# Optimization experiments

Measured on AMD Instinct MI355X. Metric: run time of the kernel, lower is better.

The kernel has to match this reference:

```python
import jax, jax.numpy as jnp
import numpy as np

N = 5000
NFEAT = 512
NHID = 64
NHEADS = 8
NCLASS = 40
ALPHA = 0.2  # leaky relu slope
NEG_INF = -9e15


def setup_inputs() -> dict:
    key = jax.random.key(0)
    ks = jax.random.split(key, 12)
    x = jax.random.normal(ks[0], (N, NFEAT), dtype=jnp.float32)
    # binary adjacency, ~32 avg degree, with self loops
    adj = (jax.random.uniform(ks[1], (N, N)) < (32.0 / N)).astype(jnp.float32)
    adj = jnp.maximum(adj, jnp.eye(N, dtype=jnp.float32))
    s = 1.0 / np.sqrt(NFEAT)
    W_h = jax.random.uniform(ks[2], (NHEADS, NFEAT, NHID), minval=-s, maxval=s, dtype=jnp.float32)
    a_h = jax.random.uniform(ks[3], (NHEADS, 2 * NHID), minval=-s, maxval=s, dtype=jnp.float32)
    s2 = 1.0 / np.sqrt(NHID * NHEADS)
    W_o = jax.random.uniform(ks[4], (NHID * NHEADS, NHID), minval=-s2, maxval=s2, dtype=jnp.float32)
    a_o = jax.random.uniform(ks[5], (2 * NHID,), minval=-s2, maxval=s2, dtype=jnp.float32)
    s3 = 1.0 / np.sqrt(NHID)
    fc1_w = jax.random.uniform(ks[6], (NHID, 200), minval=-s3, maxval=s3, dtype=jnp.float32)
    fc1_b = jax.random.uniform(ks[7], (200,), minval=-s3, maxval=s3, dtype=jnp.float32)
    s4 = 1.0 / np.sqrt(200)
    fc2_w = jax.random.uniform(ks[8], (200, NCLASS), minval=-s4, maxval=s4, dtype=jnp.float32)
    fc2_b = jax.random.uniform(ks[9], (NCLASS,), minval=-s4, maxval=s4, dtype=jnp.float32)
    return {"x": x, "adj": adj, "W_h": W_h, "a_h": a_h, "W_o": W_o, "a_o": a_o,
            "fc1_w": fc1_w, "fc1_b": fc1_b, "fc2_w": fc2_w, "fc2_b": fc2_b}


def _masked_attention(e, adj):
    # e: [..., N, N]; mask where adj == 0, then row softmax
    e = jnp.where(adj > 0, e, NEG_INF)
    return jax.nn.softmax(e, axis=-1)


def reference(x, adj, W_h, a_h, W_o, a_o, fc1_w, fc1_b, fc2_w, fc2_b):
    # ---- multi-head GAT layer (concat=True), eval mode (dropout off) ----
    Wh = jnp.einsum('nf,hfo->hno', x, W_h)                 # [H, N, nhid]
    f1 = jnp.einsum('hno,ho->hn', Wh, a_h[:, :NHID])       # [H, N]
    f2 = jnp.einsum('hno,ho->hn', Wh, a_h[:, NHID:])       # [H, N]
    e = jax.nn.leaky_relu(f1[:, :, None] + f2[:, None, :], ALPHA)  # [H, N, N]
    att = _masked_attention(e, adj[None, :, :])
    h = jnp.einsum('hnm,hmo->hno', att, Wh)                # [H, N, nhid]
    h1 = jax.nn.elu(h).transpose(1, 0, 2).reshape(N, NHEADS * NHID)  # concat heads

    # ---- output GAT layer (concat=False) ----
    Wh2 = h1 @ W_o                                         # [N, nhid]
    g1 = Wh2 @ a_o[:NHID]                                  # [N]
    g2 = Wh2 @ a_o[NHID:]                                  # [N]
    e2 = jax.nn.leaky_relu(g1[:, None] + g2[None, :], ALPHA)
    att2 = _masked_attention(e2, adj)
    h2 = att2 @ Wh2                                        # [N, nhid]

    # ---- MLP head ----
    h3 = jax.nn.elu(h2 @ fc1_w + fc1_b)
    return h3 @ fc2_w + fc2_b                              # [N, nclass]
```

## Files before the change

### kernel.cpp

```cpp
#include <hip/hip_runtime.h>

typedef unsigned short u16;
typedef unsigned int u32;
typedef __bf16 bf16_t;
typedef __bf16 bf16x8 __attribute__((ext_vector_type(8)));
typedef float f32x4 __attribute__((ext_vector_type(4)));

#define NN 5000
#define NF 512
#define NH 64
#define HEADS 8
#define NCLS 40
#define CAP 128
#define LRELU 0.2f

__device__ __forceinline__ bool adj_is_bf16(const void* adj) {
    return ((*(const u32*)adj) & 0xFFFFu) != 0u;
}
__device__ __forceinline__ u16 rne_bf16(float f) {
    u32 u = __float_as_uint(f);
    u += 0x7FFFu + ((u >> 16) & 1u);
    return (u16)(u >> 16);
}
__device__ __forceinline__ float up_bf16(u16 h) {
    return __uint_as_float((u32)h << 16);
}

#define CVT_AB_BLKS 344
__global__ __launch_bounds__(256) void prep(const void* __restrict__ x, const void* __restrict__ W_h,
                                            const void* __restrict__ adj,
                                            const void* a_h, const void* W_o, const void* a_o,
                                            const void* f1w, const void* f1b,
                                            const void* f2w, const void* f2b,
                                            u16* __restrict__ xc, u16* __restrict__ whc,
                                            float* a_hc, float* W_oc, float* a_oc,
                                            float* f1wc, float* f1bc, float* f2wc, float* f2bc,
                                            int* __restrict__ nbr, int* __restrict__ deg) {
    const bool isb = adj_is_bf16(adj);
    const int b = blockIdx.x;
    if (b < NN) {
        __shared__ int cnt;
        if (threadIdx.x == 0) cnt = 0;
        __syncthreads();
        int* nrow = nbr + (size_t)b * CAP;
        if (isb) {
            const uint4* row4 = (const uint4*)((const u16*)adj + (size_t)b * NN);
            for (int c = threadIdx.x; c < NN / 8; c += 256) {
                uint4 v = row4[c];
                u32 w[4] = {v.x, v.y, v.z, v.w};
                int base = c * 8;
                #pragma unroll
                for (int q = 0; q < 4; ++q) {
                    if (w[q] & 0xFFFFu) { int p = atomicAdd(&cnt, 1); if (p < CAP) nrow[p] = base + 2 * q; }
                    if (w[q] >> 16)     { int p = atomicAdd(&cnt, 1); if (p < CAP) nrow[p] = base + 2 * q + 1; }
                }
            }
        } else {
            const uint4* row4 = (const uint4*)((const float*)adj + (size_t)b * NN);
            for (int c = threadIdx.x; c < NN / 4; c += 256) {
                uint4 v = row4[c];
                u32 w[4] = {v.x, v.y, v.z, v.w};
                int base = c * 4;
                #pragma unroll
                for (int q = 0; q < 4; ++q)
                    if (w[q]) { int p = atomicAdd(&cnt, 1); if (p < CAP) nrow[p] = base + q; }
            }
        }
        __syncthreads();
        if (threadIdx.x == 0) deg[b] = cnt < CAP ? cnt : CAP;
    } else if (b < NN + CVT_AB_BLKS) {
        const int total = NN * NF + HEADS * NF * NH;
        for (int i = (b - NN) * 256 + threadIdx.x; i < total; i += CVT_AB_BLKS * 256) {
            const void* src; u16* dst; int off;
            if (i < NN * NF) { src = x; dst = xc; off = i; }
            else             { src = W_h; dst = whc; off = i - NN * NF; }
            dst[off] = isb ? ((const u16*)src)[off] : rne_bf16(((const float*)src)[off]);
        }
    } else {
        const int s0 = HEADS * 2 * NH, s1 = HEADS * NH * NH, s2 = 2 * NH,
                  s3 = NH * 200, s4 = 200, s5 = 200 * NCLS, s6 = NCLS;
        const int total = s0 + s1 + s2 + s3 + s4 + s5 + s6;
        for (int i = (b - NN - CVT_AB_BLKS) * 256 + threadIdx.x; i < total; i += 8 * 256) {
            const void* src; float* dst; int off = i;
            if (off < s0) { src = a_h; dst = a_hc; }
            else if ((off -= s0) < s1) { src = W_o;  dst = W_oc; }
            else if ((off -= s1) < s2) { src = a_o;  dst = a_oc; }
            else if ((off -= s2) < s3) { src = f1w;  dst = f1wc; }
            else if ((off -= s3) < s4) { src = f1b;  dst = f1bc; }
            else if ((off -= s4) < s5) { src = f2w;  dst = f2wc; }
            else { off -= s5;           src = f2b;  dst = f2bc; }
            dst[off] = isb ? up_bf16(((const u16*)src)[off]) : ((const float*)src)[off];
        }
    }
}

__global__ __launch_bounds__(256) void gemm1_f(const bf16_t* __restrict__ x,
                                               const bf16_t* __restrict__ W_h,
                                               const float* __restrict__ a_h,
                                               float* __restrict__ Wh,
                                               float* __restrict__ f1,
                                               float* __restrict__ f2) {
    const int lane = threadIdx.x & 63;
    const int wid  = threadIdx.x >> 6;
    const int rg = blockIdx.x;
    const int h  = blockIdx.y;
    const int quad = lane >> 4;
    const int lr   = lane & 15;
    const int kq   = quad * 8;
    const int nCol = wid * 16 + lr;
    const bf16_t* Bh = W_h + (size_t)h * NF * NH;
    __shared__ float f1s[4][64], f2s[4][64];

    bf16x8 bfrag[16];
    #pragma unroll
    for (int s = 0; s < 16; ++s) {
        bf16x8 bb;
        #pragma unroll
        for (int j = 0; j < 8; ++j) bb[j] = Bh[(s * 32 + kq + j) * NH + nCol];
        bfrag[s] = bb;
    }
    const float a1c = a_h[h * 128 + nCol];
    const float a2c = a_h[h * 128 + NH + nCol];

    for (int t = 0; t < 4; ++t) {
        const int rb = rg * 64 + t * 16;
        int row  = rb + lr;
        int rowc = row < NN ? row : NN - 1;
        const bf16_t* xp = x + (size_t)rowc * NF + kq;
        f32x4 acc = {0.f, 0.f, 0.f, 0.f};
        #pragma unroll
        for (int s = 0; s < 16; ++s) {
            bf16x8 a = *(const bf16x8*)(xp + s * 32);
            acc = __builtin_amdgcn_mfma_f32_16x16x32_bf16(a, bfrag[s], acc, 0, 0, 0);
        }
        #pragma unroll
        for (int r = 0; r < 4; ++r) {
            int gr = rb + quad * 4 + r;
            if (gr < NN) Wh[((size_t)(h * NN + gr)) * NH + nCol] = acc[r];
            float p1 = acc[r] * a1c, p2 = acc[r] * a2c;
            #pragma unroll
            for (int o = 8; o; o >>= 1) { p1 += __shfl_xor(p1, o); p2 += __shfl_xor(p2, o); }
            if (lr == 0) { f1s[wid][t * 16 + quad * 4 + r] = p1; f2s[wid][t * 16 + quad * 4 + r] = p2; }
        }
    }
    __syncthreads();
    if (wid == 0) {
        int gr = rg * 64 + lane;
        if (gr < NN) {
            f1[h * NN + gr] = f1s[0][lane] + f1s[1][lane] + f1s[2][lane] + f1s[3][lane];
            f2[h * NN + gr] = f2s[0][lane] + f2s[1][lane] + f2s[2][lane] + f2s[3][lane];
        }
    }
}

__global__ __launch_bounds__(256) void agg1(const float* __restrict__ Wh,
                                            const float* __restrict__ f1,
                                            const float* __restrict__ f2,
                                            const int* __restrict__ nbr,
                                            const int* __restrict__ deg,
                                            float* __restrict__ h1) {
    const int lane = threadIdx.x & 63;
    const int wid  = threadIdx.x >> 6;
    const int gw = blockIdx.x * 4 + wid;
    const int h = gw / NN;
    const int n = gw - h * NN;
    __shared__ float s_alpha[4][CAP];
    __shared__ int   s_nbr[4][CAP];
    const int d = deg[n];
    const int* nb = nbr + (size_t)n * CAP;
    const float f1n = f1[gw];
    const float* f2h = f2 + (size_t)h * NN;

    float mx = -INFINITY;
    for (int j = lane; j < d; j += 64) {
        int m = nb[j];
        s_nbr[wid][j] = m;
        float e = f1n + f2h[m];
        e = e > 0.f ? e : LRELU * e;
        s_alpha[wid][j] = e;
        mx = fmaxf(mx, e);
    }
    #pragma unroll
    for (int o = 32; o; o >>= 1) mx = fmaxf(mx, __shfl_xor(mx, o));
    float sm = 0.f;
    for (int j = lane; j < d; j += 64) {
        float p = expf(s_alpha[wid][j] - mx);
        s_alpha[wid][j] = p;
        sm += p;
    }
    #pragma unroll
    for (int o = 32; o; o >>= 1) sm += __shfl_xor(sm, o);

    float acc0 = 0.f, acc1 = 0.f;
    const float* WhL = Wh + (size_t)h * NN * NH + lane;
    int j = 0;
    for (; j + 2 <= d; j += 2) {
        acc0 += s_alpha[wid][j]     * WhL[(size_t)s_nbr[wid][j]     * NH];
        acc1 += s_alpha[wid][j + 1] * WhL[(size_t)s_nbr[wid][j + 1] * NH];
    }
    if (j < d) acc0 += s_alpha[wid][j] * WhL[(size_t)s_nbr[wid][j] * NH];
    float hv = (acc0 + acc1) / sm;
    hv = hv > 0.f ? hv : expf(hv) - 1.f;
    h1[(size_t)n * (HEADS * NH) + h * NH + lane] = hv;
}

__global__ __launch_bounds__(256) void gemm2_4(const float* __restrict__ h1,
                                               const float* __restrict__ W_o,
                                               const float* __restrict__ a_o,
                                               float* __restrict__ Wh2,
                                               float* __restrict__ g1,
                                               float* __restrict__ g2) {
    const int t = threadIdx.x;
    const int n0 = blockIdx.x * 4;
    __shared__ float sh[4 * 512];
    __shared__ float ps[4][4][64];
    const float4* src = (const float4*)(h1 + (size_t)n0 * 512);
    ((float4*)sh)[t]       = src[t];
    ((float4*)sh)[t + 256] = src[t + 256];
    __syncthreads();
    const int o = t & 63, part = t >> 6;
    float a0 = 0.f, a1 = 0.f, a2 = 0.f, a3 = 0.f;
    const float* wo = W_o + part * 128 * 64 + o;
    const float* s0 = sh + part * 128;
    #pragma unroll 4
    for (int f = 0; f < 128; ++f) {
        float w = wo[f * 64];
        a0 += s0[f] * w; a1 += s0[512 + f] * w; a2 += s0[1024 + f] * w; a3 += s0[1536 + f] * w;
    }
    ps[part][0][o] = a0; ps[part][1][o] = a1; ps[part][2][o] = a2; ps[part][3][o] = a3;
    __syncthreads();
    const int nd = t >> 6;
    float w2 = ps[0][nd][o] + ps[1][nd][o] + ps[2][nd][o] + ps[3][nd][o];
    Wh2[(size_t)(n0 + nd) * 64 + o] = w2;
    float p1 = w2 * a_o[o], p2 = w2 * a_o[64 + o];
    #pragma unroll
    for (int s = 32; s; s >>= 1) { p1 += __shfl_xor(p1, s); p2 += __shfl_xor(p2, s); }
    if (o == 0) { g1[n0 + nd] = p1; g2[n0 + nd] = p2; }
}

__global__ __launch_bounds__(256) void agg2_mlp(const float* __restrict__ Wh2,
                                                const float* __restrict__ g1,
                                                const float* __restrict__ g2,
                                                const int* __restrict__ nbr,
                                                const int* __restrict__ deg,
                                                const float* __restrict__ fc1_w,
                                                const float* __restrict__ fc1_b,
                                                const float* __restrict__ fc2_w,
                                                const float* __restrict__ fc2_b,
                                                float* __restrict__ out) {
    const int lane = threadIdx.x & 63;
    const int wid  = threadIdx.x >> 6;
    const int t = threadIdx.x;
    const int n0 = blockIdx.x * 4;
    const int n = n0 + wid;
    __shared__ float s_alpha[4][CAP];
    __shared__ int   s_nbr[4][CAP];
    __shared__ float s_h2[4][NH];
    __shared__ float s_h3[4][200];
    __shared__ float ps2[2][4][NCLS];
    const int d = deg[n];
    const int* nb = nbr + (size_t)n * CAP;
    const float gn = g1[n];

    float mx = -INFINITY;
    for (int j = lane; j < d; j += 64) {
        int m = nb[j];
        s_nbr[wid][j] = m;
        float e = gn + g2[m];
        e = e > 0.f ? e : LRELU * e;
        s_alpha[wid][j] = e;
        mx = fmaxf(mx, e);
    }
    #pragma unroll
    for (int o = 32; o; o >>= 1) mx = fmaxf(mx, __shfl_xor(mx, o));
    float sm = 0.f;
    for (int j = lane; j < d; j += 64) {
        float p = expf(s_alpha[wid][j] - mx);
        s_alpha[wid][j] = p;
        sm += p;
    }
    #pragma unroll
    for (int o = 32; o; o >>= 1) sm += __shfl_xor(sm, o);

    float acc0 = 0.f, acc1 = 0.f;
    int j = 0;
    for (; j + 2 <= d; j += 2) {
        acc0 += s_alpha[wid][j]     * Wh2[(size_t)s_nbr[wid][j]     * NH + lane];
        acc1 += s_alpha[wid][j + 1] * Wh2[(size_t)s_nbr[wid][j + 1] * NH + lane];
    }
    if (j < d) acc0 += s_alpha[wid][j] * Wh2[(size_t)s_nbr[wid][j] * NH + lane];
    s_h2[wid][lane] = (acc0 + acc1) / sm;
    __syncthreads();

    if (t < 200) {
        float b0 = 0.f, b1 = 0.f, b2 = 0.f, b3 = 0.f;
        #pragma unroll 4
        for (int f = 0; f < NH; ++f) {
            float w = fc1_w[f * 200 + t];
            b0 += s_h2[0][f] * w; b1 += s_h2[1][f] * w; b2 += s_h2[2][f] * w; b3 += s_h2[3][f] * w;
        }
        float bb = fc1_b[t];
        b0 += bb; b1 += bb; b2 += bb; b3 += bb;
        s_h3[0][t] = b0 > 0.f ? b0 : expf(b0) - 1.f;
        s_h3[1][t] = b1 > 0.f ? b1 : expf(b1) - 1.f;
        s_h3[2][t] = b2 > 0.f ? b2 : expf(b2) - 1.f;
        s_h3[3][t] = b3 > 0.f ? b3 : expf(b3) - 1.f;
    }
    __syncthreads();

    if (t < 80) {
        const int o = t % 40, fh = t / 40;
        float c0 = 0.f, c1 = 0.f, c2 = 0.f, c3 = 0.f;
        #pragma unroll 4
        for (int f = fh * 100; f < fh * 100 + 100; ++f) {
            float w = fc2_w[f * NCLS + o];
            c0 += s_h3[0][f] * w; c1 += s_h3[1][f] * w; c2 += s_h3[2][f] * w; c3 += s_h3[3][f] * w;
        }
        ps2[fh][0][o] = c0; ps2[fh][1][o] = c1; ps2[fh][2][o] = c2; ps2[fh][3][o] = c3;
    }
    __syncthreads();
    if (t < 160) {
        const int nd = t / 40, o = t % 40;
        out[(size_t)(n0 + nd) * NCLS + o] = ps2[0][nd][o] + ps2[1][nd][o] + fc2_b[o];
    }
}

extern "C" void kernel_launch(void* const* d_in, const int* in_sizes, int n_in,
                              void* d_out, int out_size, void* d_ws, size_t ws_size,
                              hipStream_t stream) {
    const void* x     = d_in[0];
    const void* adj   = d_in[1];
    const void* W_h   = d_in[2];
    const void* a_h   = d_in[3];
    const void* W_o   = d_in[4];
    const void* a_o   = d_in[5];
    const void* fc1_w = d_in[6];
    const void* fc1_b = d_in[7];
    const void* fc2_w = d_in[8];
    const void* fc2_b = d_in[9];
    float* out = (float*)d_out;

    char* ws = (char*)d_ws;
    int*   nbr   = (int*)(ws + 0);
    int*   deg   = (int*)(ws + 2560000);
    float* Wh    = (float*)(ws + 2580000);
    float* f1    = (float*)(ws + 12820000);
    float* f2    = (float*)(ws + 12980000);
    float* h1    = (float*)(ws + 13140000);
    float* Wh2   = (float*)(ws + 23380000);
    float* g1    = (float*)(ws + 24660000);
    float* g2    = (float*)(ws + 24680000);
    u16*   xc    = (u16*)(ws + 24700000);
    u16*   whc   = (u16*)(ws + 29820000);
    float* a_hc  = (float*)(ws + 30344288);
    float* W_oc  = (float*)(ws + 30348384);
    float* a_oc  = (float*)(ws + 30479456);
    float* f1wc  = (float*)(ws + 30479968);
    float* f1bc  = (float*)(ws + 30531168);
    float* f2wc  = (float*)(ws + 30531968);
    float* f2bc  = (float*)(ws + 30563968);

    prep<<<NN + CVT_AB_BLKS + 8, 256, 0, stream>>>(x, W_h, adj, a_h, W_o, a_o,
                                                   fc1_w, fc1_b, fc2_w, fc2_b,
                                                   xc, whc, a_hc, W_oc, a_oc,
                                                   f1wc, f1bc, f2wc, f2bc, nbr, deg);
    gemm1_f<<<dim3(79, HEADS), 256, 0, stream>>>((const bf16_t*)xc, (const bf16_t*)whc,
                                                 a_hc, Wh, f1, f2);
    agg1<<<HEADS * NN / 4, 256, 0, stream>>>(Wh, f1, f2, nbr, deg, h1);
    gemm2_4<<<NN / 4, 256, 0, stream>>>(h1, W_oc, a_oc, Wh2, g1, g2);
    agg2_mlp<<<NN / 4, 256, 0, stream>>>(Wh2, g1, g2, nbr, deg,
                                         f1wc, f1bc, f2wc, f2bc, out);
}
```

Baseline: 281.9 us.

## Fuse input conversion, GEMM1 and CSR build into one kernel

```diff
diff --git a/kernel.cpp b/kernel.cpp
--- a/kernel.cpp
+++ b/kernel.cpp
@@ -14,141 +14,173 @@
 #define CAP 128
 #define LRELU 0.2f
 
+#define GEMM1B (79 * HEADS)
+#define CSR_END (GEMM1B + NN)
+#define FUSED0_GRID (CSR_END + 8)
+
 __device__ __forceinline__ bool adj_is_bf16(const void* adj) {
     return ((*(const u32*)adj) & 0xFFFFu) != 0u;
 }
-__device__ __forceinline__ u16 rne_bf16(float f) {
-    u32 u = __float_as_uint(f);
-    u += 0x7FFFu + ((u >> 16) & 1u);
-    return (u16)(u >> 16);
-}
 __device__ __forceinline__ float up_bf16(u16 h) {
     return __uint_as_float((u32)h << 16);
 }
 
-#define CVT_AB_BLKS 344
-__global__ __launch_bounds__(256) void prep(const void* __restrict__ x, const void* __restrict__ W_h,
-                                            const void* __restrict__ adj,
-                                            const void* a_h, const void* W_o, const void* a_o,
-                                            const void* f1w, const void* f1b,
-                                            const void* f2w, const void* f2b,
-                                            u16* __restrict__ xc, u16* __restrict__ whc,
-                                            float* a_hc, float* W_oc, float* a_oc,
-                                            float* f1wc, float* f1bc, float* f2wc, float* f2bc,
-                                            int* __restrict__ nbr, int* __restrict__ deg) {
+__global__ __launch_bounds__(256) void fused0(const void* __restrict__ x,
+                                              const void* __restrict__ W_h,
+                                              const void* __restrict__ adj,
+                                              const void* __restrict__ a_h,
+                                              const void* W_o, const void* a_o,
+                                              const void* f1w, const void* f1b,
+                                              const void* f2w, const void* f2b,
+                                              float* __restrict__ Wh,
+                                              float* __restrict__ f1,
+                                              float* __restrict__ f2,
+                                              int* __restrict__ nbr, int* __restrict__ deg,
+                                              float* W_oc, float* a_oc,
+                                              float* f1wc, float* f1bc, float* f2wc, float* f2bc) {
     const bool isb = adj_is_bf16(adj);
     const int b = blockIdx.x;
-    if (b < NN) {
-        __shared__ int cnt;
+    __shared__ float f1s[4][64], f2s[4][64];
+    __shared__ int cnt;
+
+    if (b < GEMM1B) {
+        const int lane = threadIdx.x & 63;
+        const int wid  = threadIdx.x >> 6;
+        const int h  = b / 79;
+        const int rg = b - h * 79;
+        const int quad = lane >> 4;
+        const int lr   = lane & 15;
+        const int kq   = quad * 8;
+        const int nCol = wid * 16 + lr;
+
+        bf16x8 bfrag[16];
+        if (isb) {
+            const bf16_t* Bh = (const bf16_t*)W_h + (size_t)h * NF * NH;
+            #pragma unroll
+            for (int s = 0; s < 16; ++s) {
+                bf16x8 bb;
+                #pragma unroll
+                for (int j = 0; j < 8; ++j) bb[j] = Bh[(s * 32 + kq + j) * NH + nCol];
+                bfrag[s] = bb;
+            }
+        } else {
+            const float* Bh = (const float*)W_h + (size_t)h * NF * NH;
+            #pragma unroll
+            for (int s = 0; s < 16; ++s) {
+                bf16x8 bb;
+                #pragma unroll
+                for (int j = 0; j < 8; ++j) bb[j] = (bf16_t)Bh[(s * 32 + kq + j) * NH + nCol];
+                bfrag[s] = bb;
+            }
+        }
+        const float a1c = isb ? up_bf16(((const u16*)a_h)[h * 128 + nCol])
+                              : ((const float*)a_h)[h * 128 + nCol];
+        const float a2c = isb ? up_bf16(((const u16*)a_h)[h * 128 + NH + nCol])
+                              : ((const float*)a_h)[h * 128 + NH + nCol];
+
+        for (int t = 0; t < 4; ++t) {
+            const int rb = rg * 64 + t * 16;
+            int row  = rb + lr;
+            int rowc = row < NN ? row : NN - 1;
+            f32x4 acc = {0.f, 0.f, 0.f, 0.f};
+            if (isb) {
+                const bf16_t* xp = (const bf16_t*)x + (size_t)rowc * NF + kq;
+                #pragma unroll
+                for (int s = 0; s < 16; ++s) {
+                    bf16x8 a = *(const bf16x8*)(xp + s * 32);
+                    acc = __builtin_amdgcn_mfma_f32_16x16x32_bf16(a, bfrag[s], acc, 0, 0, 0);
+                }
+            } else {
+                const float* xp = (const float*)x + (size_t)rowc * NF + kq;
+                #pragma unroll
+                for (int s = 0; s < 16; ++s) {
+                    float4 lo = *(const float4*)(xp + s * 32);
+                    float4 hi = *(const float4*)(xp + s * 32 + 4);
+                    bf16x8 a;
+                    a[0] = (bf16_t)lo.x; a[1] = (bf16_t)lo.y; a[2] = (bf16_t)lo.z; a[3] = (bf16_t)lo.w;
+                    a[4] = (bf16_t)hi.x; a[5] = (bf16_t)hi.y; a[6] = (bf16_t)hi.z; a[7] = (bf16_t)hi.w;
+                    acc = __builtin_amdgcn_mfma_f32_16x16x32_bf16(a, bfrag[s], acc, 0, 0, 0);
+                }
+            }
+            #pragma unroll
+            for (int r = 0; r < 4; ++r) {
+                int gr = rb + quad * 4 + r;
+                if (gr < NN) Wh[((size_t)(h * NN + gr)) * NH + nCol] = acc[r];
+                float p1 = acc[r] * a1c, p2 = acc[r] * a2c;
+                #pragma unroll
+                for (int o = 8; o; o >>= 1) { p1 += __shfl_xor(p1, o); p2 += __shfl_xor(p2, o); }
+                if (lr == 0) { f1s[wid][t * 16 + quad * 4 + r] = p1; f2s[wid][t * 16 + quad * 4 + r] = p2; }
+            }
+        }
+        __syncthreads();
+        if (wid == 0) {
+            int gr = rg * 64 + lane;
+            if (gr < NN) {
+                f1[h * NN + gr] = f1s[0][lane] + f1s[1][lane] + f1s[2][lane] + f1s[3][lane];
+                f2[h * NN + gr] = f2s[0][lane] + f2s[1][lane] + f2s[2][lane] + f2s[3][lane];
+            }
+        }
+    } else if (b < CSR_END) {
+        const int n = b - GEMM1B;
         if (threadIdx.x == 0) cnt = 0;
         __syncthreads();
-        int* nrow = nbr + (size_t)b * CAP;
+        int* nrow = nbr + (size_t)n * CAP;
         if (isb) {
-            const uint4* row4 = (const uint4*)((const u16*)adj + (size_t)b * NN);
-            for (int c = threadIdx.x; c < NN / 8; c += 256) {
-                uint4 v = row4[c];
-                u32 w[4] = {v.x, v.y, v.z, v.w};
-                int base = c * 8;
-                #pragma unroll
-                for (int q = 0; q < 4; ++q) {
-                    if (w[q] & 0xFFFFu) { int p = atomicAdd(&cnt, 1); if (p < CAP) nrow[p] = base + 2 * q; }
-                    if (w[q] >> 16)     { int p = atomicAdd(&cnt, 1); if (p < CAP) nrow[p] = base + 2 * q + 1; }
+            const uint4* row4 = (const uint4*)((const u16*)adj + (size_t)n * NN);
+            uint4 v[3];
+            #pragma unroll
+            for (int k = 0; k < 3; ++k) {
+                int c = threadIdx.x + k * 256;
+                if (c < 625) v[k] = row4[c];
+            }
+            #pragma unroll
+            for (int k = 0; k < 3; ++k) {
+                int c = threadIdx.x + k * 256;
+                if (c < 625) {
+                    u32 w[4] = {v[k].x, v[k].y, v[k].z, v[k].w};
+                    int base = c * 8;
+                    #pragma unroll
+                    for (int q = 0; q < 4; ++q) {
+                        if (w[q] & 0xFFFFu) { int p = atomicAdd(&cnt, 1); if (p < CAP) nrow[p] = base + 2 * q; }
+                        if (w[q] >> 16)     { int p = atomicAdd(&cnt, 1); if (p < CAP) nrow[p] = base + 2 * q + 1; }
+                    }
                 }
             }
         } else {
-            const uint4* row4 = (const uint4*)((const float*)adj + (size_t)b * NN);
-            for (int c = threadIdx.x; c < NN / 4; c += 256) {
-                uint4 v = row4[c];
-                u32 w[4] = {v.x, v.y, v.z, v.w};
-                int base = c * 4;
-                #pragma unroll
-                for (int q = 0; q < 4; ++q)
-                    if (w[q]) { int p = atomicAdd(&cnt, 1); if (p < CAP) nrow[p] = base + q; }
+            const uint4* row4 = (const uint4*)((const float*)adj + (size_t)n * NN);
+            uint4 v[5];
+            #pragma unroll
+            for (int k = 0; k < 5; ++k) {
+                int c = threadIdx.x + k * 256;
+                if (c < 1250) v[k] = row4[c];
+            }
+            #pragma unroll
+            for (int k = 0; k < 5; ++k) {
+                int c = threadIdx.x + k * 256;
+                if (c < 1250) {
+                    u32 w[4] = {v[k].x, v[k].y, v[k].z, v[k].w};
+                    int base = c * 4;
+                    #pragma unroll
+                    for (int q = 0; q < 4; ++q)
+                        if (w[q]) { int p = atomicAdd(&cnt, 1); if (p < CAP) nrow[p] = base + q; }
+                }
             }
         }
         __syncthreads();
-        if (threadIdx.x == 0) deg[b] = cnt < CAP ? cnt : CAP;
-    } else if (b < NN + CVT_AB_BLKS) {
-        const int total = NN * NF + HEADS * NF * NH;
-        for (int i = (b - NN) * 256 + threadIdx.x; i < total; i += CVT_AB_BLKS * 256) {
-            const void* src; u16* dst; int off;
-            if (i < NN * NF) { src = x; dst = xc; off = i; }
-            else             { src = W_h; dst = whc; off = i - NN * NF; }
-            dst[off] = isb ? ((const u16*)src)[off] : rne_bf16(((const float*)src)[off]);
-        }
+        if (threadIdx.x == 0) deg[n] = cnt < CAP ? cnt : CAP;
     } else {
-        const int s0 = HEADS * 2 * NH, s1 = HEADS * NH * NH, s2 = 2 * NH,
-                  s3 = NH * 200, s4 = 200, s5 = 200 * NCLS, s6 = NCLS;
-        const int total = s0 + s1 + s2 + s3 + s4 + s5 + s6;
-        for (int i = (b - NN - CVT_AB_BLKS) * 256 + threadIdx.x; i < total; i += 8 * 256) {
+        const int s1 = HEADS * NH * NH, s2 = 2 * NH, s3 = NH * 200, s4 = 200,
+                  s5 = 200 * NCLS, s6 = NCLS;
+        const int total = s1 + s2 + s3 + s4 + s5 + s6;
+        for (int i = (b - CSR_END) * 256 + threadIdx.x; i < total; i += 8 * 256) {
             const void* src; float* dst; int off = i;
-            if (off < s0) { src = a_h; dst = a_hc; }
-            else if ((off -= s0) < s1) { src = W_o;  dst = W_oc; }
+            if (off < s1) { src = W_o; dst = W_oc; }
             else if ((off -= s1) < s2) { src = a_o;  dst = a_oc; }
             else if ((off -= s2) < s3) { src = f1w;  dst = f1wc; }
             else if ((off -= s3) < s4) { src = f1b;  dst = f1bc; }
             else if ((off -= s4) < s5) { src = f2w;  dst = f2wc; }
             else { off -= s5;           src = f2b;  dst = f2bc; }
             dst[off] = isb ? up_bf16(((const u16*)src)[off]) : ((const float*)src)[off];
-        }
-    }
-}
-
-__global__ __launch_bounds__(256) void gemm1_f(const bf16_t* __restrict__ x,
-                                               const bf16_t* __restrict__ W_h,
-                                               const float* __restrict__ a_h,
-                                               float* __restrict__ Wh,
-                                               float* __restrict__ f1,
-                                               float* __restrict__ f2) {
-    const int lane = threadIdx.x & 63;
-    const int wid  = threadIdx.x >> 6;
-    const int rg = blockIdx.x;
-    const int h  = blockIdx.y;
-    const int quad = lane >> 4;
-    const int lr   = lane & 15;
-    const int kq   = quad * 8;
-    const int nCol = wid * 16 + lr;
-    const bf16_t* Bh = W_h + (size_t)h * NF * NH;
-    __shared__ float f1s[4][64], f2s[4][64];
-
-    bf16x8 bfrag[16];
-    #pragma unroll
-    for (int s = 0; s < 16; ++s) {
-        bf16x8 bb;
-        #pragma unroll
-        for (int j = 0; j < 8; ++j) bb[j] = Bh[(s * 32 + kq + j) * NH + nCol];
-        bfrag[s] = bb;
-    }
-    const float a1c = a_h[h * 128 + nCol];
-    const float a2c = a_h[h * 128 + NH + nCol];
-
-    for (int t = 0; t < 4; ++t) {
-        const int rb = rg * 64 + t * 16;
-        int row  = rb + lr;
-        int rowc = row < NN ? row : NN - 1;
-        const bf16_t* xp = x + (size_t)rowc * NF + kq;
-        f32x4 acc = {0.f, 0.f, 0.f, 0.f};
-        #pragma unroll
-        for (int s = 0; s < 16; ++s) {
-            bf16x8 a = *(const bf16x8*)(xp + s * 32);
-            acc = __builtin_amdgcn_mfma_f32_16x16x32_bf16(a, bfrag[s], acc, 0, 0, 0);
-        }
-        #pragma unroll
-        for (int r = 0; r < 4; ++r) {
-            int gr = rb + quad * 4 + r;
-            if (gr < NN) Wh[((size_t)(h * NN + gr)) * NH + nCol] = acc[r];
-            float p1 = acc[r] * a1c, p2 = acc[r] * a2c;
-            #pragma unroll
-            for (int o = 8; o; o >>= 1) { p1 += __shfl_xor(p1, o); p2 += __shfl_xor(p2, o); }
-            if (lr == 0) { f1s[wid][t * 16 + quad * 4 + r] = p1; f2s[wid][t * 16 + quad * 4 + r] = p2; }
-        }
-    }
-    __syncthreads();
-    if (wid == 0) {
-        int gr = rg * 64 + lane;
-        if (gr < NN) {
-            f1[h * NN + gr] = f1s[0][lane] + f1s[1][lane] + f1s[2][lane] + f1s[3][lane];
-            f2[h * NN + gr] = f2s[0][lane] + f2s[1][lane] + f2s[2][lane] + f2s[3][lane];
         }
     }
 }
@@ -350,22 +382,17 @@
     float* Wh2   = (float*)(ws + 23380000);
     float* g1    = (float*)(ws + 24660000);
     float* g2    = (float*)(ws + 24680000);
-    u16*   xc    = (u16*)(ws + 24700000);
-    u16*   whc   = (u16*)(ws + 29820000);
-    float* a_hc  = (float*)(ws + 30344288);
-    float* W_oc  = (float*)(ws + 30348384);
-    float* a_oc  = (float*)(ws + 30479456);
-    float* f1wc  = (float*)(ws + 30479968);
-    float* f1bc  = (float*)(ws + 30531168);
-    float* f2wc  = (float*)(ws + 30531968);
-    float* f2bc  = (float*)(ws + 30563968);
-
-    prep<<<NN + CVT_AB_BLKS + 8, 256, 0, stream>>>(x, W_h, adj, a_h, W_o, a_o,
-                                                   fc1_w, fc1_b, fc2_w, fc2_b,
-                                                   xc, whc, a_hc, W_oc, a_oc,
-                                                   f1wc, f1bc, f2wc, f2bc, nbr, deg);
-    gemm1_f<<<dim3(79, HEADS), 256, 0, stream>>>((const bf16_t*)xc, (const bf16_t*)whc,
-                                                 a_hc, Wh, f1, f2);
+    float* W_oc  = (float*)(ws + 24700000);
+    float* a_oc  = (float*)(ws + 24831072);
+    float* f1wc  = (float*)(ws + 24831584);
+    float* f1bc  = (float*)(ws + 24882784);
+    float* f2wc  = (float*)(ws + 24883584);
+    float* f2bc  = (float*)(ws + 24915584);
+
+    fused0<<<FUSED0_GRID, 256, 0, stream>>>(x, W_h, adj, a_h, W_o, a_o,
+                                            fc1_w, fc1_b, fc2_w, fc2_b,
+                                            Wh, f1, f2, nbr, deg,
+                                            W_oc, a_oc, f1wc, f1bc, f2wc, f2bc);
     agg1<<<HEADS * NN / 4, 256, 0, stream>>>(Wh, f1, f2, nbr, deg, h1);
     gemm2_4<<<NN / 4, 256, 0, stream>>>(h1, W_oc, a_oc, Wh2, g1, g2);
     agg2_mlp<<<NN / 4, 256, 0, stream>>>(Wh2, g1, g2, nbr, deg,
```

Measured after the change: 283.9 us. Within noise of the previous version (+0.7%).

## Scan adjacency rows per wavefront with ballot compaction and unroll gathers

Applied to the files above, without the earlier changes.

```diff
diff --git a/kernel.cpp b/kernel.cpp
--- a/kernel.cpp
+++ b/kernel.cpp
@@ -2,6 +2,7 @@
 
 typedef unsigned short u16;
 typedef unsigned int u32;
+typedef unsigned long long u64;
 typedef __bf16 bf16_t;
 typedef __bf16 bf16x8 __attribute__((ext_vector_type(8)));
 typedef float f32x4 __attribute__((ext_vector_type(4)));
@@ -14,6 +15,10 @@
 #define CAP 128
 #define LRELU 0.2f
 
+#define SCAN_BLKS 1250
+#define CVT_AB_BLKS 344
+#define PREP2_GRID (SCAN_BLKS + CVT_AB_BLKS + 8)
+
 __device__ __forceinline__ bool adj_is_bf16(const void* adj) {
     return ((*(const u32*)adj) & 0xFFFFu) != 0u;
 }
@@ -26,51 +31,88 @@
     return __uint_as_float((u32)h << 16);
 }
 
-#define CVT_AB_BLKS 344
-__global__ __launch_bounds__(256) void prep(const void* __restrict__ x, const void* __restrict__ W_h,
-                                            const void* __restrict__ adj,
-                                            const void* a_h, const void* W_o, const void* a_o,
-                                            const void* f1w, const void* f1b,
-                                            const void* f2w, const void* f2b,
-                                            u16* __restrict__ xc, u16* __restrict__ whc,
-                                            float* a_hc, float* W_oc, float* a_oc,
-                                            float* f1wc, float* f1bc, float* f2wc, float* f2bc,
-                                            int* __restrict__ nbr, int* __restrict__ deg) {
+__global__ __launch_bounds__(256) void prep2(const void* __restrict__ adj,
+                                             const void* __restrict__ x, const void* __restrict__ W_h,
+                                             const void* a_h, const void* W_o, const void* a_o,
+                                             const void* f1w, const void* f1b,
+                                             const void* f2w, const void* f2b,
+                                             int* __restrict__ nbr, int* __restrict__ deg,
+                                             u16* __restrict__ xc, u16* __restrict__ whc,
+                                             float* a_hc, float* W_oc, float* a_oc,
+                                             float* f1wc, float* f1bc, float* f2wc, float* f2bc) {
     const bool isb = adj_is_bf16(adj);
     const int b = blockIdx.x;
-    if (b < NN) {
-        __shared__ int cnt;
-        if (threadIdx.x == 0) cnt = 0;
-        __syncthreads();
-        int* nrow = nbr + (size_t)b * CAP;
-        if (isb) {
-            const uint4* row4 = (const uint4*)((const u16*)adj + (size_t)b * NN);
-            for (int c = threadIdx.x; c < NN / 8; c += 256) {
-                uint4 v = row4[c];
-                u32 w[4] = {v.x, v.y, v.z, v.w};
-                int base = c * 8;
+    if (b < SCAN_BLKS) {
+        const int lane = threadIdx.x & 63;
+        const int wid  = threadIdx.x >> 6;
+        const int n = b * 4 + wid;
+        int* nrow = nbr + (size_t)n * CAP;
+        const u64 lt = (1ull << lane) - 1;
+        int total = 0;
+        if (!isb) {
+            const uint4* row4 = (const uint4*)((const float*)adj + (size_t)n * NN);
+            #pragma unroll
+            for (int pass = 0; pass < 2; ++pass) {
+                uint4 v[10];
                 #pragma unroll
-                for (int q = 0; q < 4; ++q) {
-                    if (w[q] & 0xFFFFu) { int p = atomicAdd(&cnt, 1); if (p < CAP) nrow[p] = base + 2 * q; }
-                    if (w[q] >> 16)     { int p = atomicAdd(&cnt, 1); if (p < CAP) nrow[p] = base + 2 * q + 1; }
+                for (int k = 0; k < 10; ++k) {
+                    int c = (pass * 10 + k) * 64 + lane;
+                    v[k] = (c < 1250) ? row4[c] : make_uint4(0u, 0u, 0u, 0u);
+                }
+                #pragma unroll
+                for (int k = 0; k < 10; ++k) {
+                    int c = (pass * 10 + k) * 64 + lane;
+                    u32 w[4] = {v[k].x, v[k].y, v[k].z, v[k].w};
+                    #pragma unroll
+                    for (int j = 0; j < 4; ++j) {
+                        bool nz = w[j] != 0u;
+                        u64 m = __ballot(nz);
+                        if (nz) {
+                            int pos = total + __popcll(m & lt);
+                            if (pos < CAP) nrow[pos] = c * 4 + j;
+                        }
+                        total += __popcll(m);
+                    }
                 }
             }
         } else {
-            const uint4* row4 = (const uint4*)((const float*)adj + (size_t)b * NN);
-            for (int c = threadIdx.x; c < NN / 4; c += 256) {
-                uint4 v = row4[c];
-                u32 w[4] = {v.x, v.y, v.z, v.w};
-                int base = c * 4;
+            const uint4* row4 = (const uint4*)((const u16*)adj + (size_t)n * NN);
+            #pragma unroll
+            for (int pass = 0; pass < 2; ++pass) {
+                uint4 v[5];
                 #pragma unroll
-                for (int q = 0; q < 4; ++q)
-                    if (w[q]) { int p = atomicAdd(&cnt, 1); if (p < CAP) nrow[p] = base + q; }
+                for (int k = 0; k < 5; ++k) {
+                    int c = (pass * 5 + k) * 64 + lane;
+                    v[k] = (c < 625) ? row4[c] : make_uint4(0u, 0u, 0u, 0u);
+                }
+                #pragma unroll
+                for (int k = 0; k < 5; ++k) {
+                    int c = (pass * 5 + k) * 64 + lane;
+                    u32 w[4] = {v[k].x, v[k].y, v[k].z, v[k].w};
+                    #pragma unroll
+                    for (int j = 0; j < 4; ++j) {
+                        bool nz = (w[j] & 0xFFFFu) != 0u;
+                        u64 m = __ballot(nz);
+                        if (nz) {
+                            int pos = total + __popcll(m & lt);
+                            if (pos < CAP) nrow[pos] = c * 8 + 2 * j;
+                        }
+                        total += __popcll(m);
+                        bool nz2 = (w[j] >> 16) != 0u;
+                        u64 m2 = __ballot(nz2);
+                        if (nz2) {
+                            int pos = total + __popcll(m2 & lt);
+                            if (pos < CAP) nrow[pos] = c * 8 + 2 * j + 1;
+                        }
+                        total += __popcll(m2);
+                    }
+                }
             }
         }
-        __syncthreads();
-        if (threadIdx.x == 0) deg[b] = cnt < CAP ? cnt : CAP;
-    } else if (b < NN + CVT_AB_BLKS) {
+        if (lane == 0) deg[n] = total < CAP ? total : CAP;
+    } else if (b < SCAN_BLKS + CVT_AB_BLKS) {
         const int total = NN * NF + HEADS * NF * NH;
-        for (int i = (b - NN) * 256 + threadIdx.x; i < total; i += CVT_AB_BLKS * 256) {
+        for (int i = (b - SCAN_BLKS) * 256 + threadIdx.x; i < total; i += CVT_AB_BLKS * 256) {
             const void* src; u16* dst; int off;
             if (i < NN * NF) { src = x; dst = xc; off = i; }
             else             { src = W_h; dst = whc; off = i - NN * NF; }
@@ -80,7 +122,7 @@
         const int s0 = HEADS * 2 * NH, s1 = HEADS * NH * NH, s2 = 2 * NH,
                   s3 = NH * 200, s4 = 200, s5 = 200 * NCLS, s6 = NCLS;
         const int total = s0 + s1 + s2 + s3 + s4 + s5 + s6;
-        for (int i = (b - NN - CVT_AB_BLKS) * 256 + threadIdx.x; i < total; i += 8 * 256) {
+        for (int i = (b - SCAN_BLKS - CVT_AB_BLKS) * 256 + threadIdx.x; i < total; i += 8 * 256) {
             const void* src; float* dst; int off = i;
             if (off < s0) { src = a_h; dst = a_hc; }
             else if ((off -= s0) < s1) { src = W_o;  dst = W_oc; }
@@ -191,15 +233,17 @@
     #pragma unroll
     for (int o = 32; o; o >>= 1) sm += __shfl_xor(sm, o);
 
-    float acc0 = 0.f, acc1 = 0.f;
+    float acc0 = 0.f, acc1 = 0.f, acc2 = 0.f, acc3 = 0.f;
     const float* WhL = Wh + (size_t)h * NN * NH + lane;
     int j = 0;
-    for (; j + 2 <= d; j += 2) {
+    for (; j + 4 <= d; j += 4) {
         acc0 += s_alpha[wid][j]     * WhL[(size_t)s_nbr[wid][j]     * NH];
         acc1 += s_alpha[wid][j + 1] * WhL[(size_t)s_nbr[wid][j + 1] * NH];
-    }
-    if (j < d) acc0 += s_alpha[wid][j] * WhL[(size_t)s_nbr[wid][j] * NH];
-    float hv = (acc0 + acc1) / sm;
+        acc2 += s_alpha[wid][j + 2] * WhL[(size_t)s_nbr[wid][j + 2] * NH];
+        acc3 += s_alpha[wid][j + 3] * WhL[(size_t)s_nbr[wid][j + 3] * NH];
+    }
+    for (; j < d; ++j) acc0 += s_alpha[wid][j] * WhL[(size_t)s_nbr[wid][j] * NH];
+    float hv = (acc0 + acc1 + acc2 + acc3) / sm;
     hv = hv > 0.f ? hv : expf(hv) - 1.f;
     h1[(size_t)n * (HEADS * NH) + h * NH + lane] = hv;
 }
@@ -282,14 +326,16 @@
     #pragma unroll
     for (int o = 32; o; o >>= 1) sm += __shfl_xor(sm, o);
 
-    float acc0 = 0.f, acc1 = 0.f;
+    float acc0 = 0.f, acc1 = 0.f, acc2 = 0.f, acc3 = 0.f;
     int j = 0;
-    for (; j + 2 <= d; j += 2) {
+    for (; j + 4 <= d; j += 4) {
         acc0 += s_alpha[wid][j]     * Wh2[(size_t)s_nbr[wid][j]     * NH + lane];
         acc1 += s_alpha[wid][j + 1] * Wh2[(size_t)s_nbr[wid][j + 1] * NH + lane];
-    }
-    if (j < d) acc0 += s_alpha[wid][j] * Wh2[(size_t)s_nbr[wid][j] * NH + lane];
-    s_h2[wid][lane] = (acc0 + acc1) / sm;
+        acc2 += s_alpha[wid][j + 2] * Wh2[(size_t)s_nbr[wid][j + 2] * NH + lane];
+        acc3 += s_alpha[wid][j + 3] * Wh2[(size_t)s_nbr[wid][j + 3] * NH + lane];
+    }
+    for (; j < d; ++j) acc0 += s_alpha[wid][j] * Wh2[(size_t)s_nbr[wid][j] * NH + lane];
+    s_h2[wid][lane] = (acc0 + acc1 + acc2 + acc3) / sm;
     __syncthreads();
 
     if (t < 200) {
@@ -360,10 +406,10 @@
     float* f2wc  = (float*)(ws + 30531968);
     float* f2bc  = (float*)(ws + 30563968);
 
-    prep<<<NN + CVT_AB_BLKS + 8, 256, 0, stream>>>(x, W_h, adj, a_h, W_o, a_o,
-                                                   fc1_w, fc1_b, fc2_w, fc2_b,
-                                                   xc, whc, a_hc, W_oc, a_oc,
-                                                   f1wc, f1bc, f2wc, f2bc, nbr, deg);
+    prep2<<<PREP2_GRID, 256, 0, stream>>>(adj, x, W_h, a_h, W_o, a_o,
+                                          fc1_w, fc1_b, fc2_w, fc2_b,
+                                          nbr, deg, xc, whc, a_hc, W_oc, a_oc,
+                                          f1wc, f1bc, f2wc, f2bc);
     gemm1_f<<<dim3(79, HEADS), 256, 0, stream>>>((const bf16_t*)xc, (const bf16_t*)whc,
                                                  a_hc, Wh, f1, f2);
     agg1<<<HEADS * NN / 4, 256, 0, stream>>>(Wh, f1, f2, nbr, deg, h1);
```

New measurement: 283.2 us. About the same (+0.4%).
